# Performance work log

Measured on AMD Instinct MI355X. Metric: run time of the kernel, lower is better.

Reference implementation:

```python
import jax, jax.numpy as jnp
import numpy as np

INF = 1e8
STRIDES = (8, 16, 32, 64, 128)
SIZES_OF_INTEREST = ((0.0, 80.0), (64.0, 160.0), (128.0, 320.0), (256.0, 640.0), (512.0, 1e7))
LEVEL_HW = ((128, 128), (64, 64), (32, 32), (16, 16), (8, 8))
B, N_BOX = 4, 64
MIN_RADIUS2 = 16.0          # min_radius ** 2
DELTA = (1 - 0.8) / (1 + 0.8)
ALPHA, BETA, GAMMA = 0.25, 4.0, 2.0
SIGMOID_CLAMP = 1e-4
IGNORE_HIGH_FP = 0.85
POS_W = NEG_W = 0.5
REG_WEIGHT = 1.0


def _static():
    grids, strides, ranges, loc = [], [], [], []
    for (h, w), s, (lo, hi) in zip(LEVEL_HW, STRIDES, SIZES_OF_INTEREST):
        ys, xs = np.meshgrid(np.arange(h) * s, np.arange(w) * s, indexing='ij')
        g = np.stack([xs.reshape(-1), ys.reshape(-1)], 1).astype(np.float32) + s // 2
        grids.append(g)
        strides.append(np.full(h * w, s, np.float32))
        ranges.append(np.broadcast_to(np.array([lo, hi], np.float32), (h * w, 2)).copy())
        loc.append(h * w)
    loc = np.array(loc)
    bases = np.concatenate([[0], np.cumsum(loc * B)])[:-1]
    return np.concatenate(grids), np.concatenate(strides), np.concatenate(ranges), loc, bases

_G, _S, _R, LOC_PER_LEVEL, LEVEL_BASES = _static()
GRIDS = jnp.asarray(_G)          # [M_img, 2]
STRIDE_VEC = jnp.asarray(_S)     # [M_img]
SIZE_RANGES = jnp.asarray(_R)    # [M_img, 2]
M_IMG = GRIDS.shape[0]
M_TOT = B * M_IMG


def _assign_one(boxes):
    """GT assignment for one image. boxes [N,4] -> (reg_targets [M,4], agn_hm [M])."""
    l = GRIDS[:, 0:1] - boxes[None, :, 0]
    t = GRIDS[:, 1:2] - boxes[None, :, 1]
    r = boxes[None, :, 2] - GRIDS[:, 0:1]
    b = boxes[None, :, 3] - GRIDS[:, 1:2]
    reg = jnp.stack([l, t, r, b], 2)                              # [M,N,4]
    centers = (boxes[:, :2] + boxes[:, 2:]) / 2                   # [N,2]
    s = STRIDE_VEC[:, None, None]                                 # [M,1,1]
    cdis = (centers[None] / s).astype(jnp.int32).astype(jnp.float32) * s + s / 2  # [M,N,2]
    diff = GRIDS[:, None, :] - cdis                               # [M,N,2]
    is_peak = (diff ** 2).sum(-1) == 0
    is_in = reg.min(2) > 0
    c3x3 = (jnp.abs(diff[..., 0]) <= s[..., 0]) & (jnp.abs(diff[..., 1]) <= s[..., 0]) & is_in
    crit = jnp.sqrt(((reg[:, :, :2] + reg[:, :, 2:]) ** 2).sum(2)) / 2
    cared = (crit >= SIZE_RANGES[:, 0:1]) & (crit <= SIZE_RANGES[:, 1:2])
    reg_mask = c3x3 & cared
    dist2 = ((GRIDS[:, None, :] - centers[None]) ** 2).sum(-1)
    dist2 = jnp.where(is_peak, 0.0, dist2)
    area = (boxes[:, 2] - boxes[:, 0]) * (boxes[:, 3] - boxes[:, 1])
    radius2 = jnp.maximum(DELTA ** 2 * 2 * area, MIN_RADIUS2)
    wdist2 = dist2 / radius2[None]                                # [M,N]
    d = jnp.where(reg_mask, wdist2, INF)
    min_d = d.min(1)
    min_i = d.argmin(1)
    rt = jnp.take_along_axis(reg, min_i[:, None, None], 1)[:, 0, :]
    rt = jnp.where((min_d >= INF)[:, None], -INF, rt)
    hm = jnp.exp(-wdist2.min(1))
    hm = jnp.where(hm < 1e-4, 0.0, hm)
    return rt / STRIDE_VEC[:, None], hm


def _to_level_major(x):
    """[B, M_img, ...] -> [B*M_img, ...] in level-major (level, image, loc) order == _transpose."""
    outs, start = [], 0
    for m in LOC_PER_LEVEL:
        outs.append(x[:, start:start + int(m)].reshape((B * int(m),) + x.shape[2:]))
        start += int(m)
    return jnp.concatenate(outs, 0)


def _pos_inds(boxes):
    """_get_label_inds: flat positive indices [B*N*L] plus validity mask."""
    centers = (boxes[..., :2] + boxes[..., 2:]) / 2               # [B,N,2]
    st = jnp.asarray(STRIDES, jnp.float32)
    ci = (centers[:, :, None, :] / st[None, None, :, None]).astype(jnp.int32)  # [B,N,L,2]
    Ws = jnp.asarray([w for (_, w) in LEVEL_HW])
    loc = jnp.asarray(LOC_PER_LEVEL)
    bases = jnp.asarray(LEVEL_BASES)
    im = jnp.arange(B)[:, None, None]
    pos = bases[None, None, :] + im * loc[None, None, :] + ci[..., 1] * Ws[None, None, :] + ci[..., 0]
    crit = jnp.sqrt(((boxes[..., 2:] - boxes[..., :2]) ** 2).sum(-1)) / 2     # [B,N]
    lo = jnp.asarray([r[0] for r in SIZES_OF_INTEREST])
    hi = jnp.asarray([r[1] for r in SIZES_OF_INTEREST])
    mask = (crit[..., None] >= lo) & (crit[..., None] <= hi)
    return pos.reshape(-1), mask.reshape(-1)


def _giou_loss(pred, target):
    pl, pt, pr, pb = pred[:, 0], pred[:, 1], pred[:, 2], pred[:, 3]
    tl, tt, tr, tb = target[:, 0], target[:, 1], target[:, 2], target[:, 3]
    target_area = (tl + tr) * (tt + tb)
    pred_area = (pl + pr) * (pt + pb)
    w_i = jnp.minimum(pl, tl) + jnp.minimum(pr, tr)
    g_w = jnp.maximum(pl, tl) + jnp.maximum(pr, tr)
    h_i = jnp.minimum(pb, tb) + jnp.minimum(pt, tt)
    g_h = jnp.maximum(pb, tb) + jnp.maximum(pt, tt)
    ac = g_w * g_h + 1e-7
    inter = w_i * h_i
    union = target_area + pred_area - inter
    ious = (inter + 1.0) / (union + 1.0)
    gious = ious - (ac - union) / ac
    return 1.0 - gious


def _losses(boxes, agn_hm_pred, reg_pred):
    reg_targets, hms = jax.vmap(_assign_one)(boxes)               # [B,M,4], [B,M]
    reg_targets = _to_level_major(reg_targets)                    # [M_tot,4]
    hm = _to_level_major(hms)                                     # [M_tot]
    pos_inds, pos_mask = _pos_inds(boxes)
    num_pos_avg = jnp.maximum(pos_mask.sum().astype(jnp.float32), 1.0)

    reg_valid = reg_targets.max(1) >= 0
    safe_t = jnp.where(reg_valid[:, None], reg_targets, 1.0)
    reg_norm = jnp.maximum(reg_valid.sum().astype(jnp.float32), 1.0)
    reg_loss = REG_WEIGHT * jnp.sum(jnp.where(reg_valid, _giou_loss(reg_pred, safe_t), 0.0)) / reg_norm

    # binary heatmap focal loss (class-agnostic)
    pred = jnp.clip(jax.nn.sigmoid(agn_hm_pred), SIGMOID_CLAMP, 1.0 - SIGMOID_CLAMP)
    neg_w = jnp.power(1.0 - hm, BETA)
    idx = jnp.clip(pos_inds, 0, M_TOT - 1)
    pos_pred = pred[idx]
    pos_terms = jnp.where(pos_mask, jnp.log(pos_pred) * jnp.power(1.0 - pos_pred, GAMMA), 0.0)
    neg_terms = jnp.log(1.0 - pred) * jnp.power(pred, GAMMA) * neg_w
    neg_terms = jnp.where(pred < IGNORE_HIGH_FP, neg_terms, 0.0)
    agn_pos = POS_W * (ALPHA * (-pos_terms.sum())) / num_pos_avg
    agn_neg = NEG_W * ((1.0 - ALPHA) * (-neg_terms.sum())) / num_pos_avg
    return jnp.stack([reg_loss, agn_pos, agn_neg])


def setup_inputs() -> dict:
    key = jax.random.key(0)
    k1, k2, k3, k4, k5 = jax.random.split(key, 5)
    cxy = jax.random.uniform(k1, (B, N_BOX, 2), minval=40.0, maxval=984.0)
    wh = jax.random.uniform(k2, (B, N_BOX, 2), minval=16.0, maxval=512.0)
    boxes = jnp.concatenate([jnp.clip(cxy - wh / 2, 0.0, 1024.0),
                             jnp.clip(cxy + wh / 2, 0.0, 1024.0)], -1)
    gt_classes = jax.random.randint(k3, (B, N_BOX), 0, 4)
    agn_hm_pred = jax.random.normal(k4, (M_TOT,), jnp.float32) * 2.0 - 3.0
    reg_pred = jax.random.uniform(k5, (M_TOT, 4), jnp.float32) * 6.0 + 0.1
    return {"boxes": boxes, "gt_classes": gt_classes,
            "agn_hm_pred": agn_hm_pred, "reg_pred": reg_pred}


def reference(boxes, gt_classes, agn_hm_pred, reg_pred):
    # gt_classes unused: only_proposal=True -> class-agnostic heatmap path
    return _losses(boxes, agn_hm_pred, reg_pred)
```

## Files before the change

kernel.cpp:

```cpp
#include <hip/hip_runtime.h>
#include <math.h>

#define M_TOT 87296
#define NMAIN 682
#define INF_F 100000000.0f


__global__ __launch_bounds__(256, 2) void main_kernel(
    const float* __restrict__ boxes,
    const float* __restrict__ agn,
    const float* __restrict__ reg_pred,
    float* __restrict__ ws)
{
    __shared__ float4 sBox[256];
    __shared__ float  sRed[16];

    const int t   = threadIdx.x;
    const int blk = blockIdx.x;

    const int   LB_[5]   = {0, 65536, 81920, 86016, 87040};
    const int   locSh[5] = {14, 12, 10, 8, 6};
    const int   wSh[5]   = {7, 6, 5, 4, 3};
    const float SV[5]    = {8.f, 16.f, 32.f, 64.f, 128.f};
    const float LOv[5]   = {0.f, 64.f, 128.f, 256.f, 512.f};
    const float HIv[5]   = {80.f, 160.f, 320.f, 640.f, 10000000.f};

    if (blk == NMAIN) {
        const int   LOC[5] = {16384, 4096, 1024, 256, 64};
        const int   WW[5]  = {128, 64, 32, 16, 8};
        float psum = 0.f, pcnt = 0.f;
        for (int j = t; j < 1280; j += 256) {
            const int lev = j % 5;
            const int bn  = j / 5;
            const int b   = bn >> 6;
            const float4 bx = ((const float4*)boxes)[bn];
            const float cx = (bx.x + bx.z) * 0.5f;
            const float cy = (bx.y + bx.w) * 0.5f;
            const int cix = (int)(cx / SV[lev]);
            const int ciy = (int)(cy / SV[lev]);
            int pos = LB_[lev] + b * LOC[lev] + ciy * WW[lev] + cix;
            pos = min(max(pos, 0), M_TOT - 1);
            const float dx = bx.z - bx.x, dy = bx.w - bx.y;
            const float crit = sqrtf(dx * dx + dy * dy) * 0.5f;
            const bool msk = (crit >= LOv[lev]) && (crit <= HIv[lev]);
            const float z = agn[pos];
            float pp = 1.0f / (1.0f + expf(-z));
            pp = fminf(fmaxf(pp, 1e-4f), 1.0f - 1e-4f);
            if (msk) {
                const float om = 1.0f - pp;
                psum += logf(pp) * (om * om);
                pcnt += 1.0f;
            }
        }
        for (int off = 32; off; off >>= 1) {
            psum += __shfl_down(psum, off);
            pcnt += __shfl_down(pcnt, off);
        }
        if ((t & 63) == 0) { sRed[t >> 6] = psum; sRed[4 + (t >> 6)] = pcnt; }
        __syncthreads();
        if (t == 0) {
            ws[3 * NMAIN]     = sRed[0] + sRed[1] + sRed[2] + sRed[3];
            ws[3 * NMAIN + 1] = sRed[4] + sRed[5] + sRed[6] + sRed[7];
        }
        return;
    }

    const int mbase = blk << 7;
    int lev;
    if      (mbase < 65536) lev = 0;
    else if (mbase < 81920) lev = 1;
    else if (mbase < 86016) lev = 2;
    else if (mbase < 87040) lev = 3;
    else                    lev = 4;

    const int   LB    = LB_[lev];
    const int   lsh   = locSh[lev];
    const int   wsh   = wSh[lev];
    const float s     = SV[lev];
    const float inv_s = 1.0f / s;
    const float half  = 0.5f * s;
    const float lo    = LOv[lev], hi = HIv[lev];

    sBox[t] = ((const float4*)boxes)[t];
    __syncthreads();

    const int g       = t >> 3;
    const int su      = t & 7;
    const int locBase = mbase + g * 4;
    const int imgBase = ((locBase - LB) >> lsh) << 6;

    const double DELTA = (1.0 - 0.8) / (1.0 + 0.8);
    const float  RADC  = (float)(DELTA * DELTA * 2.0);

    float bx1[8], by1[8], bx2[8], by2[8], bcx[8], bcy[8], bqx[8], bqy[8], bir[8];
    int caredMask = 0;
    #pragma unroll
    for (int k = 0; k < 8; ++k) {
        const float4 A = sBox[imgBase + su + 8 * k];
        bx1[k] = A.x; by1[k] = A.y; bx2[k] = A.z; by2[k] = A.w;
        bcx[k] = (A.x + A.z) * 0.5f;
        bcy[k] = (A.y + A.w) * 0.5f;
        bqx[k] = truncf(bcx[k] * inv_s) * s + half;
        bqy[k] = truncf(bcy[k] * inv_s) * s + half;
        const float area = (A.z - A.x) * (A.w - A.y);
        bir[k] = 1.0f / fmaxf(RADC * area, 16.0f);
        const float bw = A.z - A.x, bh = A.w - A.y;
        const float crit = sqrtf(bw * bw + bh * bh) * 0.5f;
        caredMask |= ((crit >= lo) && (crit <= hi)) ? (1 << k) : 0;
    }

    float minW[4], bestD[4];
    int   bestN[4];
    #pragma unroll
    for (int j = 0; j < 4; ++j) { minW[j] = INF_F; bestD[j] = INF_F; bestN[j] = 0; }

    #pragma unroll
    for (int j = 0; j < 4; ++j) {
        const int   p  = (locBase + j - LB) & ((1 << lsh) - 1);
        const float gx = (float)(p & ((1 << wsh) - 1)) * s + half;
        const float gy = (float)(p >> wsh) * s + half;
        #pragma unroll
        for (int k = 0; k < 8; ++k) {
            const float l  = gx - bx1[k];
            const float tt = gy - by1[k];
            const float rr = bx2[k] - gx;
            const float bb = by2[k] - gy;
            const bool is_in = fminf(fminf(l, tt), fminf(rr, bb)) > 0.0f;
            const float dx = gx - bqx[k], dy = gy - bqy[k];
            const bool is_peak = (dx * dx + dy * dy) == 0.0f;
            const bool msk = (fabsf(dx) <= s) && (fabsf(dy) <= s) && is_in
                             && ((caredMask >> k) & 1);
            const float ddx = gx - bcx[k], ddy = gy - bcy[k];
            const float dist2 = is_peak ? 0.0f : (ddx * ddx + ddy * ddy);
            const float w2 = dist2 * bir[k];
            minW[j] = fminf(minW[j], w2);
            const float d = msk ? w2 : INF_F;
            if (d < bestD[j]) { bestD[j] = d; bestN[j] = su + 8 * k; }
        }
    }

    unsigned long long myKey = ~0ULL; float myMinW = INF_F;
    #pragma unroll
    for (int j = 0; j < 4; ++j) {
        unsigned long long kj =
            ((unsigned long long)__float_as_uint(bestD[j]) << 6) | (unsigned)bestN[j];
        float wj = minW[j];
        #pragma unroll
        for (int m = 1; m < 8; m <<= 1) {
            const unsigned long long o = __shfl_xor(kj, m);
            kj = o < kj ? o : kj;
            wj = fminf(wj, __shfl_xor(wj, m));
        }
        if (su == j) { myKey = kj; myMinW = wj; }
    }

    float neg_term = 0.f, reg_term = 0.f, reg_val = 0.f;
    if (su < 4) {
        const int myloc = locBase + su;
        float hmv = expf(-myMinW);
        if (hmv < 1e-4f) hmv = 0.0f;
        const float u = 1.0f - hmv;
        const float neg_w = (u * u) * (u * u);
        const float z = agn[myloc];
        float pr = 1.0f / (1.0f + expf(-z));
        pr = fminf(fmaxf(pr, 1e-4f), 1.0f - 1e-4f);
        if (pr < 0.85f) neg_term = logf(1.0f - pr) * (pr * pr) * neg_w;

        if ((unsigned)(myKey >> 6) < __float_as_uint(INF_F)) {
            reg_val = 1.0f;
            const int n = (int)(myKey & 63);
            const float4 A = sBox[imgBase + n];
            const int   p  = (myloc - LB) & ((1 << lsh) - 1);
            const float gx = (float)(p & ((1 << wsh) - 1)) * s + half;
            const float gy = (float)(p >> wsh) * s + half;
            const float tl  = (gx - A.x) * inv_s;
            const float tt2 = (gy - A.y) * inv_s;
            const float tr  = (A.z - gx) * inv_s;
            const float tb  = (A.w - gy) * inv_s;
            const float4 pv = ((const float4*)reg_pred)[myloc];
            const float pl = pv.x, pt = pv.y, prr = pv.z, pb = pv.w;
            const float target_area = (tl + tr) * (tt2 + tb);
            const float pred_area   = (pl + prr) * (pt + pb);
            const float w_i = fminf(pl, tl) + fminf(prr, tr);
            const float g_w = fmaxf(pl, tl) + fmaxf(prr, tr);
            const float h_i = fminf(pb, tb) + fminf(pt, tt2);
            const float g_h = fmaxf(pb, tb) + fmaxf(pt, tt2);
            const float ac    = g_w * g_h + 1e-7f;
            const float inter = w_i * h_i;
            const float uni   = target_area + pred_area - inter;
            const float ious  = (inter + 1.0f) / (uni + 1.0f);
            const float gious = ious - (ac - uni) / ac;
            reg_term = 1.0f - gious;
        }
    }

    float r0 = reg_term, r1 = reg_val, r2 = neg_term;
    for (int off = 32; off; off >>= 1) {
        r0 += __shfl_down(r0, off);
        r1 += __shfl_down(r1, off);
        r2 += __shfl_down(r2, off);
    }
    if ((t & 63) == 0) {
        const int w = t >> 6;
        sRed[w * 3 + 0] = r0; sRed[w * 3 + 1] = r1; sRed[w * 3 + 2] = r2;
    }
    __syncthreads();
    if (t == 0) {
        ws[blk]             = sRed[0] + sRed[3] + sRed[6] + sRed[9];
        ws[NMAIN + blk]     = sRed[1] + sRed[4] + sRed[7] + sRed[10];
        ws[2 * NMAIN + blk] = sRed[2] + sRed[5] + sRed[8] + sRed[11];
    }
}

__global__ __launch_bounds__(256) void finalize(
    const float* __restrict__ ws,
    float* __restrict__ out)
{
    const int t = threadIdx.x;
    float racc = 0.f, cacc = 0.f, nacc = 0.f;
    for (int j = t; j < NMAIN; j += 256) {
        racc += ws[j];
        cacc += ws[NMAIN + j];
        nacc += ws[2 * NMAIN + j];
    }
    for (int off = 32; off; off >>= 1) {
        racc += __shfl_down(racc, off);
        cacc += __shfl_down(cacc, off);
        nacc += __shfl_down(nacc, off);
    }
    __shared__ float sr[4][3];
    if ((t & 63) == 0) {
        const int w = t >> 6;
        sr[w][0] = racc; sr[w][1] = cacc; sr[w][2] = nacc;
    }
    __syncthreads();
    if (t == 0) {
        const float RS = sr[0][0] + sr[1][0] + sr[2][0] + sr[3][0];
        const float RC = sr[0][1] + sr[1][1] + sr[2][1] + sr[3][1];
        const float NS = sr[0][2] + sr[1][2] + sr[2][2] + sr[3][2];
        const float PS = ws[3 * NMAIN];
        const float PC = ws[3 * NMAIN + 1];
        const float num_pos  = fmaxf(PC, 1.0f);
        const float reg_norm = fmaxf(RC, 1.0f);
        out[0] = RS / reg_norm;
        out[1] = 0.5f * (0.25f * -PS) / num_pos;
        out[2] = 0.5f * (0.75f * -NS) / num_pos;
    }
}

extern "C" void kernel_launch(void* const* d_in, const int* in_sizes, int n_in,
                              void* d_out, int out_size, void* d_ws, size_t ws_size,
                              hipStream_t stream) {
    const float* boxes    = (const float*)d_in[0];
    const float* agn      = (const float*)d_in[2];
    const float* reg_pred = (const float*)d_in[3];
    float* out = (float*)d_out;
    float* ws  = (float*)d_ws;

    main_kernel<<<NMAIN + 1, 256, 0, stream>>>(boxes, agn, reg_pred, ws);
    finalize<<<1, 256, 0, stream>>>(ws, out);
}
```

Baseline: 69.27 us.

## Hoist per-box y terms out of location loop and prefetch inputs early

The inner assignment loop is reordered to iterate boxes outside and the four consecutive x-locations inside. All y-dependent terms (top/bottom inside test, y-distance squared, y-window and peak checks) are precomputed once per box, and x terms become base value plus j*s. The agn and reg_pred loads are issued before the box loop so their latency overlaps the compute, and launch bounds rise to 3 blocks per SIMD to raise occupancy. This relies on the four locations sharing a row, and rewriting the peak test as dx==0 && dy==0 may differ from the original squared-sum test at the bit level. The higher block count may also force register spilling.

```diff
diff --git a/kernel.cpp b/kernel.cpp
--- a/kernel.cpp
+++ b/kernel.cpp
@@ -6,7 +6,7 @@
 #define INF_F 100000000.0f
 
 
-__global__ __launch_bounds__(256, 2) void main_kernel(
+__global__ __launch_bounds__(256, 3) void main_kernel(
     const float* __restrict__ boxes,
     const float* __restrict__ agn,
     const float* __restrict__ reg_pred,
@@ -88,25 +88,45 @@
     const int su      = t & 7;
     const int locBase = mbase + g * 4;
     const int imgBase = ((locBase - LB) >> lsh) << 6;
+    const int p0      = (locBase - LB) & ((1 << lsh) - 1);
+    const float gx0   = (float)(p0 & ((1 << wsh) - 1)) * s + half;
+    const float gy    = (float)(p0 >> wsh) * s + half;
+
+    float  zEarly  = 0.f;
+    float4 pvEarly = make_float4(0.f, 0.f, 0.f, 0.f);
+    if (su < 4) {
+        zEarly  = agn[locBase + su];
+        pvEarly = ((const float4*)reg_pred)[locBase + su];
+    }
 
     const double DELTA = (1.0 - 0.8) / (1.0 + 0.8);
     const float  RADC  = (float)(DELTA * DELTA * 2.0);
 
-    float bx1[8], by1[8], bx2[8], by2[8], bcx[8], bcy[8], bqx[8], bqy[8], bir[8];
-    int caredMask = 0;
+    float l0[8], rr0[8], ttbb[8], dx0[8], ddx0[8], ddy2[8], bir[8];
+    bool  yok[8], ypk[8];
     #pragma unroll
     for (int k = 0; k < 8; ++k) {
         const float4 A = sBox[imgBase + su + 8 * k];
-        bx1[k] = A.x; by1[k] = A.y; bx2[k] = A.z; by2[k] = A.w;
-        bcx[k] = (A.x + A.z) * 0.5f;
-        bcy[k] = (A.y + A.w) * 0.5f;
-        bqx[k] = truncf(bcx[k] * inv_s) * s + half;
-        bqy[k] = truncf(bcy[k] * inv_s) * s + half;
-        const float area = (A.z - A.x) * (A.w - A.y);
+        const float bcx = (A.x + A.z) * 0.5f;
+        const float bcy = (A.y + A.w) * 0.5f;
+        const float bqx = truncf(bcx * inv_s) * s + half;
+        const float bqy = truncf(bcy * inv_s) * s + half;
+        l0[k]  = gx0 - A.x;
+        rr0[k] = A.z - gx0;
+        const float tt = gy - A.y;
+        const float bb = A.w - gy;
+        ttbb[k] = fminf(tt, bb);
+        dx0[k]  = gx0 - bqx;
+        const float dyc = gy - bqy;
+        ddx0[k] = gx0 - bcx;
+        const float ddy = gy - bcy;
+        ddy2[k] = ddy * ddy;
+        const float bw = A.z - A.x, bh = A.w - A.y;
+        const float area = bw * bh;
         bir[k] = 1.0f / fmaxf(RADC * area, 16.0f);
-        const float bw = A.z - A.x, bh = A.w - A.y;
         const float crit = sqrtf(bw * bw + bh * bh) * 0.5f;
-        caredMask |= ((crit >= lo) && (crit <= hi)) ? (1 << k) : 0;
+        yok[k] = (fabsf(dyc) <= s) && (crit >= lo) && (crit <= hi);
+        ypk[k] = (dyc == 0.0f);
     }
 
     float minW[4], bestD[4];
@@ -115,27 +135,30 @@
     for (int j = 0; j < 4; ++j) { minW[j] = INF_F; bestD[j] = INF_F; bestN[j] = 0; }
 
     #pragma unroll
-    for (int j = 0; j < 4; ++j) {
-        const int   p  = (locBase + j - LB) & ((1 << lsh) - 1);
-        const float gx = (float)(p & ((1 << wsh) - 1)) * s + half;
-        const float gy = (float)(p >> wsh) * s + half;
+    for (int k = 0; k < 8; ++k) {
+        const float tb  = ttbb[k];
+        const float b_  = bir[k];
+        const float dy2 = ddy2[k];
+        const bool  yk  = yok[k];
+        const bool  pk  = ypk[k];
+        const int   n   = su + 8 * k;
         #pragma unroll
-        for (int k = 0; k < 8; ++k) {
-            const float l  = gx - bx1[k];
-            const float tt = gy - by1[k];
-            const float rr = bx2[k] - gx;
-            const float bb = by2[k] - gy;
-            const bool is_in = fminf(fminf(l, tt), fminf(rr, bb)) > 0.0f;
-            const float dx = gx - bqx[k], dy = gy - bqy[k];
-            const bool is_peak = (dx * dx + dy * dy) == 0.0f;
-            const bool msk = (fabsf(dx) <= s) && (fabsf(dy) <= s) && is_in
-                             && ((caredMask >> k) & 1);
-            const float ddx = gx - bcx[k], ddy = gy - bcy[k];
-            const float dist2 = is_peak ? 0.0f : (ddx * ddx + ddy * ddy);
-            const float w2 = dist2 * bir[k];
+        for (int j = 0; j < 4; ++j) {
+            const float js  = (float)j * s;
+            const float l   = l0[k] + js;
+            const float rr  = rr0[k] - js;
+            const float dx  = dx0[k] + js;
+            const float ddx = ddx0[k] + js;
+            const bool is_in = fminf(fminf(l, rr), tb) > 0.0f;
+            const bool xok   = fabsf(dx) <= s;
+            const bool peak  = (dx == 0.0f) && pk;
+            const bool msk   = is_in && xok && yk;
+            float dist2 = ddx * ddx + dy2;
+            dist2 = peak ? 0.0f : dist2;
+            const float w2 = dist2 * b_;
             minW[j] = fminf(minW[j], w2);
             const float d = msk ? w2 : INF_F;
-            if (d < bestD[j]) { bestD[j] = d; bestN[j] = su + 8 * k; }
+            if (d < bestD[j]) { bestD[j] = d; bestN[j] = n; }
         }
     }
 
@@ -156,13 +179,11 @@
 
     float neg_term = 0.f, reg_term = 0.f, reg_val = 0.f;
     if (su < 4) {
-        const int myloc = locBase + su;
         float hmv = expf(-myMinW);
         if (hmv < 1e-4f) hmv = 0.0f;
         const float u = 1.0f - hmv;
         const float neg_w = (u * u) * (u * u);
-        const float z = agn[myloc];
-        float pr = 1.0f / (1.0f + expf(-z));
+        float pr = 1.0f / (1.0f + expf(-zEarly));
         pr = fminf(fmaxf(pr, 1e-4f), 1.0f - 1e-4f);
         if (pr < 0.85f) neg_term = logf(1.0f - pr) * (pr * pr) * neg_w;
 
@@ -170,21 +191,19 @@
             reg_val = 1.0f;
             const int n = (int)(myKey & 63);
             const float4 A = sBox[imgBase + n];
-            const int   p  = (myloc - LB) & ((1 << lsh) - 1);
-            const float gx = (float)(p & ((1 << wsh) - 1)) * s + half;
-            const float gy = (float)(p >> wsh) * s + half;
+            const int   px = (p0 & ((1 << wsh) - 1)) + su;
+            const float gx = (float)px * s + half;
             const float tl  = (gx - A.x) * inv_s;
             const float tt2 = (gy - A.y) * inv_s;
             const float tr  = (A.z - gx) * inv_s;
-            const float tb  = (A.w - gy) * inv_s;
-            const float4 pv = ((const float4*)reg_pred)[myloc];
-            const float pl = pv.x, pt = pv.y, prr = pv.z, pb = pv.w;
-            const float target_area = (tl + tr) * (tt2 + tb);
+            const float tb2 = (A.w - gy) * inv_s;
+            const float pl = pvEarly.x, pt = pvEarly.y, prr = pvEarly.z, pb = pvEarly.w;
+            const float target_area = (tl + tr) * (tt2 + tb2);
             const float pred_area   = (pl + prr) * (pt + pb);
             const float w_i = fminf(pl, tl) + fminf(prr, tr);
             const float g_w = fmaxf(pl, tl) + fmaxf(prr, tr);
-            const float h_i = fminf(pb, tb) + fminf(pt, tt2);
-            const float g_h = fmaxf(pb, tb) + fmaxf(pt, tt2);
+            const float h_i = fminf(pb, tb2) + fminf(pt, tt2);
+            const float g_h = fmaxf(pb, tb2) + fmaxf(pt, tt2);
             const float ac    = g_w * g_h + 1e-7f;
             const float inter = w_i * h_i;
             const float uni   = target_area + pred_area - inter;
```

After: 70.02 us (median of 2 runs). About the same (+1.1%).
